# Performance work log

Hardware: AMD Instinct MI355X
Metric: run time of the kernel (lower is better)

## Reference

```python
import jax, jax.numpy as jnp
import numpy as np

C = 1.0      # base manifold curvature (Lorentz c)
C_E = 1.0    # expert manifold curvature (all experts init to c=1.0)
K = 1        # n_activated_experts (top-k)
SCALE = 2.0  # LResNet scale for shared-expert combine
EPS = 1e-8


def _lorentz_swiglu(x, W1, W3, W2, c_mid, c_out, prescale):
    """LorentzExpert / LorentzFeedForward: SwiGLU on space coords with Lorentz time lift.
    x: [T, D] (full Lorentz vector). W1,W3: [I-1, D]; W2: [D-1, I]. Returns [T, D]."""
    if prescale:
        x = x * np.float32(np.sqrt(C_E / C))  # x * sqrt(c_expert / c)
    s1 = jax.nn.silu(x @ W1.T)                 # [T, I-1] w1(x, return_space=True)
    s3 = x @ W3.T                              # [T, I-1] w3(x, return_space=True)
    sp = s1 * s3                               # gated space part
    t = jnp.sqrt(jnp.clip((sp * sp).sum(-1, keepdims=True) + c_mid, EPS))
    h = jnp.concatenate([t, sp], axis=-1)      # [T, I] point on expert manifold
    o = h @ W2.T                               # [T, D-1] w2 space output
    ot = jnp.sqrt(jnp.clip((o * o).sum(-1, keepdims=True) + c_out, EPS))
    return jnp.concatenate([ot, o], axis=-1)   # [T, D] on base manifold


def setup_inputs() -> dict:
    key = jax.random.key(0)
    ks = jax.random.split(key, 9)
    T, D, E, I = 2048, 1024, 8, 1024
    x = jax.random.normal(ks[0], (T, D), jnp.float32)
    gate_w = jax.random.normal(ks[1], (E, D - 1), jnp.float32) / np.sqrt(D - 1)
    gate_b = jax.random.normal(ks[2], (E,), jnp.float32) * 0.01
    W1 = jax.random.normal(ks[3], (E, I - 1, D), jnp.float32) / np.sqrt(D)
    W3 = jax.random.normal(ks[4], (E, I - 1, D), jnp.float32) / np.sqrt(D)
    W2 = jax.random.normal(ks[5], (E, D - 1, I), jnp.float32) / np.sqrt(I)
    Ws1 = jax.random.normal(ks[6], (I - 1, D), jnp.float32) / np.sqrt(D)
    Ws3 = jax.random.normal(ks[7], (I - 1, D), jnp.float32) / np.sqrt(D)
    Ws2 = jax.random.normal(ks[8], (D - 1, I), jnp.float32) / np.sqrt(I)
    return {"x": x, "gate_w": gate_w, "gate_b": gate_b, "W1": W1, "W3": W3,
            "W2": W2, "Ws1": Ws1, "Ws3": Ws3, "Ws2": Ws2}


def reference(x, gate_w, gate_b, W1, W3, W2, Ws1, Ws3, Ws2):
    T, D = x.shape
    E = gate_w.shape[0]
    # ---- Gate (softmax scoring, n_groups == 1, route_scale == 1.0) ----
    logits = x[:, 1:] @ gate_w.T                                    # [T, E]
    scores = jax.nn.softmax(logits.astype(jnp.float32), axis=-1)
    biased = scores + gate_b                                        # bias only affects routing
    _, idx = jax.lax.top_k(biased, K)                               # [T, K]
    weights = jnp.take_along_axis(scores, idx, axis=-1).astype(x.dtype)  # [T, K]
    # dense per-token expert gate weights [T, E]
    oh = jax.nn.one_hot(idx, E, dtype=x.dtype)                      # [T, K, E]
    gw = (oh * weights[..., None]).sum(axis=1)                      # [T, E]
    # ---- y init: project(zeros) -> [sqrt(c), 0, ..., 0] ----
    y0 = jnp.concatenate([jnp.full((T, 1), np.sqrt(C), x.dtype),
                          jnp.zeros((T, D - 1), x.dtype)], axis=-1)
    # ---- routed experts (dense reference: every expert on every token, masked combine) ----
    e_out = jax.vmap(lambda w1, w3, w2: _lorentz_swiglu(x, w1, w3, w2, C_E, C, True))(W1, W3, W2)  # [E, T, D]
    y = y0 + jnp.einsum('te,etd->td', gw, e_out)
    # ---- shared expert (LorentzFeedForward, stays on base manifold) ----
    z = _lorentz_swiglu(x, Ws1, Ws3, Ws2, C, C, False)
    # ---- LResNet weighted sum: normalize (z + scale*y) back to manifold ----
    comb = z + SCALE * y
    li = (comb[:, 1:] ** 2).sum(-1, keepdims=True) - comb[:, :1] ** 2  # Lorentz inner <comb,comb>
    out = np.float32(np.sqrt(C)) * comb / jnp.sqrt(jnp.clip(jnp.abs(li), EPS))
    return out
```

## Files before the change

kernel.cpp:

```cpp
#include <hip/hip_runtime.h>

typedef __bf16 bf16;
typedef __attribute__((ext_vector_type(8))) __bf16 bf16x8;
typedef __attribute__((ext_vector_type(4))) float floatx4;

#define TOK 2048
#define DD  1024
#define NE  8
#define S1MAX 48
#define S2MAX 80

#define MFMA16(A,B,C) __builtin_amdgcn_mfma_f32_16x16x32_bf16(A,B,C,0,0,0)

__device__ __forceinline__ void load_lds16(const bf16* g, bf16* l) {
  __builtin_amdgcn_global_load_lds(
      (const __attribute__((address_space(1))) void*)g,
      (__attribute__((address_space(3))) void*)l, 16, 0, 0);
}

__device__ __forceinline__ uint4 pack_bf8(float4 a, float4 b) {
  union { bf16 h[8]; uint4 u; } p;
  p.h[0] = (bf16)a.x; p.h[1] = (bf16)a.y; p.h[2] = (bf16)a.z; p.h[3] = (bf16)a.w;
  p.h[4] = (bf16)b.x; p.h[5] = (bf16)b.y; p.h[6] = (bf16)b.z; p.h[7] = (bf16)b.w;
  return p.u;
}

#define NCVT (8*2046 + 2046 + 8*1023 + 1023)
__global__ __launch_bounds__(128) void convert_kernel(
    const float* __restrict__ W1, const float* __restrict__ W3,
    const float* __restrict__ W2, const float* __restrict__ Ws1,
    const float* __restrict__ Ws3, const float* __restrict__ Ws2,
    bf16* __restrict__ w13, bf16* __restrict__ ws13,
    bf16* __restrict__ w2b, bf16* __restrict__ ws2b)
{
  const int r = blockIdx.x, tid = threadIdx.x;
  const float* src; bf16* dst;
  if (r < 8 * 2046) {
    const int e = r / 2046, q = r % 2046;
    src = ((q & 1) ? W3 : W1) + ((size_t)e * 1023 + (q >> 1)) * 1024;
    dst = w13 + (size_t)r * 1024;
  } else if (r < 8 * 2046 + 2046) {
    const int q = r - 8 * 2046;
    src = ((q & 1) ? Ws3 : Ws1) + (size_t)(q >> 1) * 1024;
    dst = ws13 + (size_t)q * 1024;
  } else if (r < 8 * 2046 + 2046 + 8 * 1023) {
    const int q = r - (8 * 2046 + 2046);
    src = W2 + (size_t)q * 1024;
    dst = w2b + (size_t)q * 1024;
  } else {
    const int q = r - (8 * 2046 + 2046 + 8 * 1023);
    src = Ws2 + (size_t)q * 1024;
    dst = ws2b + (size_t)q * 1024;
  }
  const float4 f0 = ((const float4*)src)[tid * 2];
  const float4 f1 = ((const float4*)src)[tid * 2 + 1];
  ((uint4*)dst)[tid] = pack_bf8(f0, f1);
}

__global__ __launch_bounds__(256) void gate_cvt_kernel(
    const float* __restrict__ x, const float* __restrict__ gate_w,
    const float* __restrict__ gate_b, bf16* __restrict__ x_bf,
    int* __restrict__ eidx, float* __restrict__ ewgt, float* __restrict__ ss)
{
  const int t = blockIdx.x, tid = threadIdx.x;
  if (tid < 4) ss[tid * TOK + t] = 0.f;
  const float4 v = ((const float4*)(x + (size_t)t * DD))[tid];
  union { bf16 h[4]; uint2 u; } pk;
  pk.h[0] = (bf16)v.x; pk.h[1] = (bf16)v.y; pk.h[2] = (bf16)v.z; pk.h[3] = (bf16)v.w;
  ((uint2*)(x_bf + (size_t)t * DD))[tid] = pk.u;

  float acc[NE];
#pragma unroll
  for (int e = 0; e < NE; ++e) acc[e] = 0.f;
  const float vv[4] = {v.x, v.y, v.z, v.w};
#pragma unroll
  for (int i = 0; i < 4; ++i) {
    const int d = tid * 4 + i;
    if (d >= 1) {
#pragma unroll
      for (int e = 0; e < NE; ++e) acc[e] += vv[i] * gate_w[e * (DD - 1) + d - 1];
    }
  }
#pragma unroll
  for (int off = 32; off > 0; off >>= 1) {
#pragma unroll
    for (int e = 0; e < NE; ++e) acc[e] += __shfl_down(acc[e], off);
  }
  __shared__ float red[4][NE];
  const int wid = tid >> 6, lane = tid & 63;
  if (lane == 0) {
#pragma unroll
    for (int e = 0; e < NE; ++e) red[wid][e] = acc[e];
  }
  __syncthreads();
  if (tid == 0) {
    float lg[NE];
#pragma unroll
    for (int e = 0; e < NE; ++e) lg[e] = red[0][e] + red[1][e] + red[2][e] + red[3][e];
    float m = lg[0];
    for (int e = 1; e < NE; ++e) m = fmaxf(m, lg[e]);
    float ex[NE], s = 0.f;
    for (int e = 0; e < NE; ++e) { ex[e] = expf(lg[e] - m); s += ex[e]; }
    const float inv = 1.f / s;
    int best = 0; float bb = ex[0] * inv + gate_b[0];
    for (int e = 1; e < NE; ++e) {
      const float b = ex[e] * inv + gate_b[e];
      if (b > bb) { bb = b; best = e; }
    }
    eidx[t] = best;
    ewgt[t] = ex[best] * inv;
  }
}

__global__ __launch_bounds__(256) void route_kernel(
    const int* __restrict__ eidx, int* __restrict__ perm,
    int* __restrict__ pos_of, int4* __restrict__ wl1, int* __restrict__ n1,
    int4* __restrict__ wl2, int* __restrict__ n2)
{
  __shared__ int cnt[NE], off[NE], bas[NE + 1];
  const int tid = threadIdx.x;
  if (tid < NE) cnt[tid] = 0;
  __syncthreads();
  for (int t = tid; t < TOK; t += 256) atomicAdd(&cnt[eidx[t]], 1);
  __syncthreads();
  if (tid == 0) {
    int run = 0;
    for (int e = 0; e < NE; ++e) { bas[e] = run; off[e] = run; run += cnt[e]; }
    bas[NE] = run;
    int n = 0;
    for (int e = 0; e < NE; ++e)
      for (int r0 = 0; r0 < cnt[e]; r0 += 128) {
        int rows = cnt[e] - r0; if (rows > 128) rows = 128;
        wl1[n++] = make_int4(bas[e] + r0, rows, e, 0);
      }
    for (int r0 = 0; r0 < TOK; r0 += 128) wl1[n++] = make_int4(r0, 128, NE, 0);
    *n1 = n;
    n = 0;
    for (int e = 0; e < NE; ++e)
      for (int r0 = 0; r0 < cnt[e]; r0 += 64) {
        int rows = cnt[e] - r0; if (rows > 64) rows = 64;
        wl2[n++] = make_int4(bas[e] + r0, rows, e, 0);
      }
    for (int r0 = 0; r0 < TOK; r0 += 64) wl2[n++] = make_int4(r0, 64, NE, 0);
    *n2 = n;
  }
  __syncthreads();
  for (int t = tid; t < TOK; t += 256) {
    const int e = eidx[t];
    const int p = atomicAdd(&off[e], 1);
    perm[p] = t;
    pos_of[t] = p;
  }
}

__global__ __launch_bounds__(256) void mlp1_kernel(
    const bf16* __restrict__ x_bf, const bf16* __restrict__ w13,
    const bf16* __restrict__ ws13,
    const int* __restrict__ perm, const int4* __restrict__ wl,
    const int* __restrict__ wl_n,
    bf16* __restrict__ h_r, bf16* __restrict__ h_s,
    float* __restrict__ ss_r, float* __restrict__ ss_z)
{
  const int bid = blockIdx.x;
  const int slot = bid >> 4, nt = bid & 15;
  if (slot >= *wl_n) return;
  const int4 wle = wl[slot];
  const int mbase = wle.x, rows = wle.y, eid = wle.z;
  const int tid = threadIdx.x;
  const bool routed = (eid < NE);
  const bf16* bmat = routed ? w13 + (size_t)eid * 2046 * 1024 : ws13;
  bf16* hbuf  = routed ? h_r : h_s;
  float* ssbuf = routed ? ss_r : ss_z;

  __shared__ __align__(16) bf16 As[128 * 64];
  __shared__ __align__(16) bf16 Bs[128 * 64];
  __shared__ int toks[128];
  if (tid < 128) {
    int r = tid < rows ? tid : rows - 1;
    toks[tid] = routed ? perm[mbase + r] : (mbase + r);
  }
  __syncthreads();

  const int wid = tid >> 6, lane = tid & 63;
  const int srow = lane >> 3;
  const int kbg  = (lane & 7) ^ (srow & 7);
  const bf16 *aG0, *aG1, *aG2, *aG3, *bG0, *bG1, *bG2, *bG3;
  bf16 *aL0, *aL1, *aL2, *aL3, *bL0, *bL1, *bL2, *bL3;
  {
    const int r0 = wid * 32;
    aG0 = x_bf + (size_t)toks[r0 +  0 + srow] * 1024 + kbg * 8;
    aG1 = x_bf + (size_t)toks[r0 +  8 + srow] * 1024 + kbg * 8;
    aG2 = x_bf + (size_t)toks[r0 + 16 + srow] * 1024 + kbg * 8;
    aG3 = x_bf + (size_t)toks[r0 + 24 + srow] * 1024 + kbg * 8;
    aL0 = As + (r0 +  0) * 64; aL1 = As + (r0 +  8) * 64;
    aL2 = As + (r0 + 16) * 64; aL3 = As + (r0 + 24) * 64;
    int b0 = nt * 128 + r0 + 0 + srow;  if (b0 > 2045) b0 = 2045;
    int b1 = nt * 128 + r0 + 8 + srow;  if (b1 > 2045) b1 = 2045;
    int b2 = nt * 128 + r0 + 16 + srow; if (b2 > 2045) b2 = 2045;
    int b3 = nt * 128 + r0 + 24 + srow; if (b3 > 2045) b3 = 2045;
    bG0 = bmat + (size_t)b0 * 1024 + kbg * 8;
    bG1 = bmat + (size_t)b1 * 1024 + kbg * 8;
    bG2 = bmat + (size_t)b2 * 1024 + kbg * 8;
    bG3 = bmat + (size_t)b3 * 1024 + kbg * 8;
    bL0 = Bs + (r0 +  0) * 64; bL1 = Bs + (r0 +  8) * 64;
    bL2 = Bs + (r0 + 16) * 64; bL3 = Bs + (r0 + 24) * 64;
  }

  const int lrow = lane & 15, quad = lane >> 4, sw = lane & 7;
  const int wrow = (wid >> 1) * 64, wcol = (wid & 1) * 64;
  int aoff[4], boff[4], koff[2];
#pragma unroll
  for (int mi = 0; mi < 4; ++mi) aoff[mi] = (wrow + mi * 16 + lrow) * 64;
#pragma unroll
  for (int ni = 0; ni < 4; ++ni) boff[ni] = (wcol + ni * 16 + lrow) * 64;
#pragma unroll
  for (int kk = 0; kk < 2; ++kk) koff[kk] = ((kk * 4 + quad) ^ sw) * 8;

  const floatx4 fz = {0.f, 0.f, 0.f, 0.f};
  floatx4 acc[4][4];
#pragma unroll
  for (int mi = 0; mi < 4; ++mi)
#pragma unroll
    for (int ni = 0; ni < 4; ++ni) acc[mi][ni] = fz;

  for (int ke = 0; ke < 1024; ke += 64) {
    load_lds16(aG0 + ke, aL0); load_lds16(aG1 + ke, aL1);
    load_lds16(aG2 + ke, aL2); load_lds16(aG3 + ke, aL3);
    load_lds16(bG0 + ke, bL0); load_lds16(bG1 + ke, bL1);
    load_lds16(bG2 + ke, bL2); load_lds16(bG3 + ke, bL3);
    __syncthreads();
#pragma unroll
    for (int kk = 0; kk < 2; ++kk) {
      bf16x8 av[4], bv[4];
#pragma unroll
      for (int mi = 0; mi < 4; ++mi) av[mi] = *(const bf16x8*)(As + aoff[mi] + koff[kk]);
#pragma unroll
      for (int ni = 0; ni < 4; ++ni) bv[ni] = *(const bf16x8*)(Bs + boff[ni] + koff[kk]);
#pragma unroll
      for (int mi = 0; mi < 4; ++mi)
#pragma unroll
        for (int ni = 0; ni < 4; ++ni)
          acc[mi][ni] = MFMA16(av[mi], bv[ni], acc[mi][ni]);
    }
    __syncthreads();
  }

#pragma unroll
  for (int mi = 0; mi < 4; ++mi) {
#pragma unroll
    for (int r = 0; r < 4; ++r) {
      const int row = wrow + mi * 16 + quad * 4 + r;
      const bool rowok = row < rows;
      float ssum = 0.f;
#pragma unroll
      for (int ni = 0; ni < 4; ++ni) {
        const float c = acc[mi][ni][r];
        const float partner = __shfl_xor(c, 1);
        const float s1 = (lane & 1) ? partner : c;
        const float s3 = (lane & 1) ? c : partner;
        const float sp = (s1 / (1.f + __expf(-s1))) * s3;
        const int P = (nt * 128 + wcol + ni * 16 + lrow) >> 1;
        const bool ok = rowok && ((lane & 1) == 0) && (P < 1023);
        if (ok) hbuf[(size_t)(mbase + row) * 1024 + 1 + P] = (bf16)sp;
        ssum += ok ? sp * sp : 0.f;
      }
      ssum += __shfl_xor(ssum, 1);
      ssum += __shfl_xor(ssum, 2);
      ssum += __shfl_xor(ssum, 4);
      ssum += __shfl_xor(ssum, 8);
      if (lrow == 0 && rowok) atomicAdd(ssbuf + mbase + row, ssum);
    }
  }
}

__global__ __launch_bounds__(256) void finalize_t_kernel(
    const float* __restrict__ ss_r, const float* __restrict__ ss_z,
    bf16* __restrict__ h_r, bf16* __restrict__ h_s)
{
  const int i = blockIdx.x * 256 + threadIdx.x;
  if (i < TOK) {
    h_r[(size_t)i * 1024] = (bf16)sqrtf(ss_r[i] + 1.0f);
    h_s[(size_t)i * 1024] = (bf16)sqrtf(ss_z[i] + 1.0f);
  }
}

__global__ __launch_bounds__(256) void mlp2_kernel(
    const bf16* __restrict__ h_r, const bf16* __restrict__ h_s,
    const bf16* __restrict__ w2b, const bf16* __restrict__ ws2b,
    const int4* __restrict__ wl, const int* __restrict__ wl_n,
    float* __restrict__ o_r, float* __restrict__ o_s,
    float* __restrict__ ss_or, float* __restrict__ ss_oz)
{
  const int bid = blockIdx.x;
  const int slot = bid >> 3, nt = bid & 7;
  if (slot >= *wl_n) return;
  const int4 wle = wl[slot];
  const int mbase = wle.x, rows = wle.y, eid = wle.z;
  const int tid = threadIdx.x;
  const bool routed = (eid < NE);
  const bf16* abuf = routed ? h_r : h_s;
  const bf16* bmat = routed ? w2b + (size_t)eid * 1023 * 1024 : ws2b;
  float* obuf  = routed ? o_r : o_s;
  float* ssbuf = routed ? ss_or : ss_oz;
  const int n0 = nt * 128;

  __shared__ __align__(16) bf16 As[64 * 64];
  __shared__ __align__(16) bf16 Bs[128 * 64];

  const int wid = tid >> 6, lane = tid & 63;
  const int srow = lane >> 3;
  const int kbg  = (lane & 7) ^ (srow & 7);
  const bf16 *aG0, *aG1, *bG0, *bG1, *bG2, *bG3;
  bf16 *aL0, *aL1, *bL0, *bL1, *bL2, *bL3;
  {
    int ra0 = wid * 16 + 0 + srow; if (ra0 >= rows) ra0 = rows - 1;
    int ra1 = wid * 16 + 8 + srow; if (ra1 >= rows) ra1 = rows - 1;
    aG0 = abuf + (size_t)(mbase + ra0) * 1024 + kbg * 8;
    aG1 = abuf + (size_t)(mbase + ra1) * 1024 + kbg * 8;
    aL0 = As + (wid * 16 + 0) * 64;
    aL1 = As + (wid * 16 + 8) * 64;
    const int r0 = wid * 32;
    int b0 = n0 + r0 + 0 + srow;  if (b0 > 1022) b0 = 1022;
    int b1 = n0 + r0 + 8 + srow;  if (b1 > 1022) b1 = 1022;
    int b2 = n0 + r0 + 16 + srow; if (b2 > 1022) b2 = 1022;
    int b3 = n0 + r0 + 24 + srow; if (b3 > 1022) b3 = 1022;
    bG0 = bmat + (size_t)b0 * 1024 + kbg * 8;
    bG1 = bmat + (size_t)b1 * 1024 + kbg * 8;
    bG2 = bmat + (size_t)b2 * 1024 + kbg * 8;
    bG3 = bmat + (size_t)b3 * 1024 + kbg * 8;
    bL0 = Bs + (r0 +  0) * 64; bL1 = Bs + (r0 +  8) * 64;
    bL2 = Bs + (r0 + 16) * 64; bL3 = Bs + (r0 + 24) * 64;
  }

  const int lrow = lane & 15, quad = lane >> 4, sw = lane & 7;
  const int wrow = (wid >> 1) * 32, wcol = (wid & 1) * 64;
  int aoff[2], boff[4], koff[2];
#pragma unroll
  for (int mi = 0; mi < 2; ++mi) aoff[mi] = (wrow + mi * 16 + lrow) * 64;
#pragma unroll
  for (int ni = 0; ni < 4; ++ni) boff[ni] = (wcol + ni * 16 + lrow) * 64;
#pragma unroll
  for (int kk = 0; kk < 2; ++kk) koff[kk] = ((kk * 4 + quad) ^ sw) * 8;

  const floatx4 fz = {0.f, 0.f, 0.f, 0.f};
  floatx4 acc[2][4];
#pragma unroll
  for (int mi = 0; mi < 2; ++mi)
#pragma unroll
    for (int ni = 0; ni < 4; ++ni) acc[mi][ni] = fz;

  for (int ke = 0; ke < 1024; ke += 64) {
    load_lds16(aG0 + ke, aL0); load_lds16(aG1 + ke, aL1);
    load_lds16(bG0 + ke, bL0); load_lds16(bG1 + ke, bL1);
    load_lds16(bG2 + ke, bL2); load_lds16(bG3 + ke, bL3);
    __syncthreads();
#pragma unroll
    for (int kk = 0; kk < 2; ++kk) {
      bf16x8 av[2], bv[4];
#pragma unroll
      for (int mi = 0; mi < 2; ++mi) av[mi] = *(const bf16x8*)(As + aoff[mi] + koff[kk]);
#pragma unroll
      for (int ni = 0; ni < 4; ++ni) bv[ni] = *(const bf16x8*)(Bs + boff[ni] + koff[kk]);
#pragma unroll
      for (int mi = 0; mi < 2; ++mi)
#pragma unroll
        for (int ni = 0; ni < 4; ++ni)
          acc[mi][ni] = MFMA16(av[mi], bv[ni], acc[mi][ni]);
    }
    __syncthreads();
  }

#pragma unroll
  for (int mi = 0; mi < 2; ++mi) {
#pragma unroll
    for (int r = 0; r < 4; ++r) {
      const int row = wrow + mi * 16 + quad * 4 + r;
      const bool rowok = row < rows;
      float ssum = 0.f;
#pragma unroll
      for (int ni = 0; ni < 4; ++ni) {
        const float v = acc[mi][ni][r];
        const int n = n0 + wcol + ni * 16 + lrow;
        const bool ok = rowok && (n < 1023);
        if (ok) obuf[(size_t)(mbase + row) * 1024 + n] = v;
        ssum += ok ? v * v : 0.f;
      }
      ssum += __shfl_xor(ssum, 1);
      ssum += __shfl_xor(ssum, 2);
      ssum += __shfl_xor(ssum, 4);
      ssum += __shfl_xor(ssum, 8);
      if (lrow == 0 && rowok) atomicAdd(ssbuf + mbase + row, ssum);
    }
  }
}

__global__ __launch_bounds__(256) void combine_kernel(
    const float* __restrict__ o_r, const float* __restrict__ o_s,
    const float* __restrict__ ss_or, const float* __restrict__ ss_oz,
    const int* __restrict__ pos_of, const float* __restrict__ wgt,
    float* __restrict__ out)
{
  const int t = blockIdx.x, tid = threadIdx.x;
  const int p = pos_of[t];
  const float w = wgt[t];
  const float4 oz = ((const float4*)(o_s + (size_t)t * 1024))[tid];
  const float4 oe = ((const float4*)(o_r + (size_t)p * 1024))[tid];
  const float tw = 2.f * w;
  float c0 = oz.x + tw * oe.x;
  float c1 = oz.y + tw * oe.y;
  float c2 = oz.z + tw * oe.z;
  float c3 = (tid == 255) ? 0.f : (oz.w + tw * oe.w);
  float ssum = c0 * c0 + c1 * c1 + c2 * c2 + c3 * c3;
#pragma unroll
  for (int off = 32; off > 0; off >>= 1) ssum += __shfl_down(ssum, off);
  __shared__ float rs[4];
  if ((tid & 63) == 0) rs[tid >> 6] = ssum;
  __syncthreads();
  const float space2 = rs[0] + rs[1] + rs[2] + rs[3];
  const float comb0 = sqrtf(ss_oz[t] + 1.f) + 2.f + 2.f * w * sqrtf(ss_or[p] + 1.f);
  const float li = space2 - comb0 * comb0;
  const float inv = 1.f / sqrtf(fmaxf(fabsf(li), 1e-8f));
  float* orow = out + (size_t)t * 1024;
  const int j = 1 + tid * 4;
  orow[j]     = c0 * inv;
  orow[j + 1] = c1 * inv;
  orow[j + 2] = c2 * inv;
  if (tid != 255) orow[j + 3] = c3 * inv;
  if (tid == 0) orow[0] = comb0 * inv;
}

extern "C" void kernel_launch(void* const* d_in, const int* in_sizes, int n_in,
                              void* d_out, int out_size, void* d_ws, size_t ws_size,
                              hipStream_t stream) {
  const float* x      = (const float*)d_in[0];
  const float* gate_w = (const float*)d_in[1];
  const float* gate_b = (const float*)d_in[2];
  const float* W1     = (const float*)d_in[3];
  const float* W3     = (const float*)d_in[4];
  const float* W2     = (const float*)d_in[5];
  const float* Ws1    = (const float*)d_in[6];
  const float* Ws3    = (const float*)d_in[7];
  const float* Ws2    = (const float*)d_in[8];
  float* out = (float*)d_out;

  char* ws = (char*)d_ws;
  size_t off = 0;
  auto alloc = [&](size_t bytes) {
    void* p = ws + off;
    off += (bytes + 255) & ~(size_t)255;
    return p;
  };
  bf16*  x_bf = (bf16*) alloc((size_t)TOK * 1024 * 2);
  bf16*  h_r  = (bf16*) alloc((size_t)TOK * 1024 * 2);
  bf16*  h_s  = (bf16*) alloc((size_t)TOK * 1024 * 2);
  float* o_r  = (float*)alloc((size_t)TOK * 1024 * 4);
  float* o_s  = (float*)alloc((size_t)TOK * 1024 * 4);
  float* ss   = (float*)alloc((size_t)4 * TOK * 4);
  int*   eidx = (int*)  alloc((size_t)TOK * 4);
  float* ewgt = (float*)alloc((size_t)TOK * 4);
  int*   perm = (int*)  alloc((size_t)TOK * 4);
  int*   posf = (int*)  alloc((size_t)TOK * 4);
  int4*  wl1  = (int4*) alloc((size_t)S1MAX * 16);
  int4*  wl2  = (int4*) alloc((size_t)S2MAX * 16);
  int*   wn   = (int*)  alloc(32);
  bf16*  w13  = (bf16*) alloc((size_t)8 * 2046 * 1024 * 2);
  bf16*  ws13 = (bf16*) alloc((size_t)2046 * 1024 * 2);
  bf16*  w2b  = (bf16*) alloc((size_t)8 * 1023 * 1024 * 2);
  bf16*  ws2b = (bf16*) alloc((size_t)1023 * 1024 * 2);

  float* ss_r  = ss;
  float* ss_z  = ss + TOK;
  float* ss_or = ss + 2 * TOK;
  float* ss_oz = ss + 3 * TOK;

  convert_kernel<<<NCVT, 128, 0, stream>>>(W1, W3, W2, Ws1, Ws3, Ws2,
                                           w13, ws13, w2b, ws2b);
  gate_cvt_kernel<<<TOK, 256, 0, stream>>>(x, gate_w, gate_b, x_bf, eidx, ewgt, ss);
  route_kernel<<<1, 256, 0, stream>>>(eidx, perm, posf, wl1, wn, wl2, wn + 1);
  mlp1_kernel<<<S1MAX * 16, 256, 0, stream>>>(x_bf, w13, ws13, perm, wl1, wn,
                                              h_r, h_s, ss_r, ss_z);
  finalize_t_kernel<<<8, 256, 0, stream>>>(ss_r, ss_z, h_r, h_s);
  mlp2_kernel<<<S2MAX * 8, 256, 0, stream>>>(h_r, h_s, w2b, ws2b, wl2, wn + 1,
                                             o_r, o_s, ss_or, ss_oz);
  combine_kernel<<<TOK, 256, 0, stream>>>(o_r, o_s, ss_or, ss_oz, posf, ewgt, out);
}
```

Measured before the change: 252.6 us.

## Double-buffer LDS tiles in both expert GEMMs with vmcnt-based waits

Both grouped GEMM kernels now keep two LDS buffers for the A and B tiles. The next K-slice is issued via global_load_lds while the current slice is consumed by MFMAs, and a raw s_waitcnt vmcnt plus s_barrier replaces the full syncthreads pair. This aims to hide global load latency behind compute. In exchange it doubles LDS use (64KB in the first kernel), which can reduce occupancy, and its correctness relies on the hand-written vmcnt counts and on the compiler not reordering the memory operations.

```diff
diff --git a/kernel.cpp b/kernel.cpp
--- a/kernel.cpp
+++ b/kernel.cpp
@@ -17,6 +17,9 @@
       (const __attribute__((address_space(1))) void*)g,
       (__attribute__((address_space(3))) void*)l, 16, 0, 0);
 }
+
+#define WBAR(N) asm volatile("s_waitcnt vmcnt(" #N ")\n\ts_barrier" ::: "memory")
+#define BARO    asm volatile("s_barrier" ::: "memory")
 
 __device__ __forceinline__ uint4 pack_bf8(float4 a, float4 b) {
   union { bf16 h[8]; uint4 u; } p;
@@ -172,8 +175,8 @@
   bf16* hbuf  = routed ? h_r : h_s;
   float* ssbuf = routed ? ss_r : ss_z;
 
-  __shared__ __align__(16) bf16 As[128 * 64];
-  __shared__ __align__(16) bf16 Bs[128 * 64];
+  __shared__ __align__(16) bf16 As[2][128 * 64];
+  __shared__ __align__(16) bf16 Bs[2][128 * 64];
   __shared__ int toks[128];
   if (tid < 128) {
     int r = tid < rows ? tid : rows - 1;
@@ -185,15 +188,15 @@
   const int srow = lane >> 3;
   const int kbg  = (lane & 7) ^ (srow & 7);
   const bf16 *aG0, *aG1, *aG2, *aG3, *bG0, *bG1, *bG2, *bG3;
-  bf16 *aL0, *aL1, *aL2, *aL3, *bL0, *bL1, *bL2, *bL3;
+  int aL0o, aL1o, aL2o, aL3o, bL0o, bL1o, bL2o, bL3o;
   {
     const int r0 = wid * 32;
     aG0 = x_bf + (size_t)toks[r0 +  0 + srow] * 1024 + kbg * 8;
     aG1 = x_bf + (size_t)toks[r0 +  8 + srow] * 1024 + kbg * 8;
     aG2 = x_bf + (size_t)toks[r0 + 16 + srow] * 1024 + kbg * 8;
     aG3 = x_bf + (size_t)toks[r0 + 24 + srow] * 1024 + kbg * 8;
-    aL0 = As + (r0 +  0) * 64; aL1 = As + (r0 +  8) * 64;
-    aL2 = As + (r0 + 16) * 64; aL3 = As + (r0 + 24) * 64;
+    aL0o = (r0 +  0) * 64; aL1o = (r0 +  8) * 64;
+    aL2o = (r0 + 16) * 64; aL3o = (r0 + 24) * 64;
     int b0 = nt * 128 + r0 + 0 + srow;  if (b0 > 2045) b0 = 2045;
     int b1 = nt * 128 + r0 + 8 + srow;  if (b1 > 2045) b1 = 2045;
     int b2 = nt * 128 + r0 + 16 + srow; if (b2 > 2045) b2 = 2045;
@@ -202,8 +205,8 @@
     bG1 = bmat + (size_t)b1 * 1024 + kbg * 8;
     bG2 = bmat + (size_t)b2 * 1024 + kbg * 8;
     bG3 = bmat + (size_t)b3 * 1024 + kbg * 8;
-    bL0 = Bs + (r0 +  0) * 64; bL1 = Bs + (r0 +  8) * 64;
-    bL2 = Bs + (r0 + 16) * 64; bL3 = Bs + (r0 + 24) * 64;
+    bL0o = (r0 +  0) * 64; bL1o = (r0 +  8) * 64;
+    bL2o = (r0 + 16) * 64; bL3o = (r0 + 24) * 64;
   }
 
   const int lrow = lane & 15, quad = lane >> 4, sw = lane & 7;
@@ -223,27 +226,39 @@
 #pragma unroll
     for (int ni = 0; ni < 4; ++ni) acc[mi][ni] = fz;
 
-  for (int ke = 0; ke < 1024; ke += 64) {
-    load_lds16(aG0 + ke, aL0); load_lds16(aG1 + ke, aL1);
-    load_lds16(aG2 + ke, aL2); load_lds16(aG3 + ke, aL3);
-    load_lds16(bG0 + ke, bL0); load_lds16(bG1 + ke, bL1);
-    load_lds16(bG2 + ke, bL2); load_lds16(bG3 + ke, bL3);
-    __syncthreads();
-#pragma unroll
-    for (int kk = 0; kk < 2; ++kk) {
-      bf16x8 av[4], bv[4];
-#pragma unroll
-      for (int mi = 0; mi < 4; ++mi) av[mi] = *(const bf16x8*)(As + aoff[mi] + koff[kk]);
-#pragma unroll
-      for (int ni = 0; ni < 4; ++ni) bv[ni] = *(const bf16x8*)(Bs + boff[ni] + koff[kk]);
-#pragma unroll
-      for (int mi = 0; mi < 4; ++mi)
-#pragma unroll
-        for (int ni = 0; ni < 4; ++ni)
-          acc[mi][ni] = MFMA16(av[mi], bv[ni], acc[mi][ni]);
-    }
-    __syncthreads();
-  }
+#define STAGE1(KE, BUF) { \
+    load_lds16(aG0 + (KE), As[BUF] + aL0o); load_lds16(aG1 + (KE), As[BUF] + aL1o); \
+    load_lds16(aG2 + (KE), As[BUF] + aL2o); load_lds16(aG3 + (KE), As[BUF] + aL3o); \
+    load_lds16(bG0 + (KE), Bs[BUF] + bL0o); load_lds16(bG1 + (KE), Bs[BUF] + bL1o); \
+    load_lds16(bG2 + (KE), Bs[BUF] + bL2o); load_lds16(bG3 + (KE), Bs[BUF] + bL3o); }
+
+#define COMP1(BUF) { \
+_Pragma("unroll") \
+    for (int kk = 0; kk < 2; ++kk) { \
+      bf16x8 av[4], bv[4]; \
+_Pragma("unroll") \
+      for (int mi = 0; mi < 4; ++mi) av[mi] = *(const bf16x8*)(As[BUF] + aoff[mi] + koff[kk]); \
+_Pragma("unroll") \
+      for (int ni = 0; ni < 4; ++ni) bv[ni] = *(const bf16x8*)(Bs[BUF] + boff[ni] + koff[kk]); \
+_Pragma("unroll") \
+      for (int mi = 0; mi < 4; ++mi) \
+_Pragma("unroll") \
+        for (int ni = 0; ni < 4; ++ni) \
+          acc[mi][ni] = MFMA16(av[mi], bv[ni], acc[mi][ni]); \
+    } }
+
+  STAGE1(0, 0)
+  STAGE1(64, 1)
+#pragma unroll 1
+  for (int t = 0; t < 7; ++t) {
+    const int ke = t * 128;
+    WBAR(8); COMP1(0) BARO; STAGE1(ke + 128, 0)
+    WBAR(8); COMP1(1) BARO; STAGE1(ke + 192, 1)
+  }
+  WBAR(8); COMP1(0)
+  WBAR(0); COMP1(1)
+#undef STAGE1
+#undef COMP1
 
 #pragma unroll
   for (int mi = 0; mi < 4; ++mi) {
@@ -304,21 +319,21 @@
   float* ssbuf = routed ? ss_or : ss_oz;
   const int n0 = nt * 128;
 
-  __shared__ __align__(16) bf16 As[64 * 64];
-  __shared__ __align__(16) bf16 Bs[128 * 64];
+  __shared__ __align__(16) bf16 As[2][64 * 64];
+  __shared__ __align__(16) bf16 Bs[2][128 * 64];
 
   const int wid = tid >> 6, lane = tid & 63;
   const int srow = lane >> 3;
   const int kbg  = (lane & 7) ^ (srow & 7);
   const bf16 *aG0, *aG1, *bG0, *bG1, *bG2, *bG3;
-  bf16 *aL0, *aL1, *bL0, *bL1, *bL2, *bL3;
+  int aL0o, aL1o, bL0o, bL1o, bL2o, bL3o;
   {
     int ra0 = wid * 16 + 0 + srow; if (ra0 >= rows) ra0 = rows - 1;
     int ra1 = wid * 16 + 8 + srow; if (ra1 >= rows) ra1 = rows - 1;
     aG0 = abuf + (size_t)(mbase + ra0) * 1024 + kbg * 8;
     aG1 = abuf + (size_t)(mbase + ra1) * 1024 + kbg * 8;
-    aL0 = As + (wid * 16 + 0) * 64;
-    aL1 = As + (wid * 16 + 8) * 64;
+    aL0o = (wid * 16 + 0) * 64;
+    aL1o = (wid * 16 + 8) * 64;
     const int r0 = wid * 32;
     int b0 = n0 + r0 + 0 + srow;  if (b0 > 1022) b0 = 1022;
     int b1 = n0 + r0 + 8 + srow;  if (b1 > 1022) b1 = 1022;
@@ -328,8 +343,8 @@
     bG1 = bmat + (size_t)b1 * 1024 + kbg * 8;
     bG2 = bmat + (size_t)b2 * 1024 + kbg * 8;
     bG3 = bmat + (size_t)b3 * 1024 + kbg * 8;
-    bL0 = Bs + (r0 +  0) * 64; bL1 = Bs + (r0 +  8) * 64;
-    bL2 = Bs + (r0 + 16) * 64; bL3 = Bs + (r0 + 24) * 64;
+    bL0o = (r0 +  0) * 64; bL1o = (r0 +  8) * 64;
+    bL2o = (r0 + 16) * 64; bL3o = (r0 + 24) * 64;
   }
 
   const int lrow = lane & 15, quad = lane >> 4, sw = lane & 7;
@@ -349,26 +364,38 @@
 #pragma unroll
     for (int ni = 0; ni < 4; ++ni) acc[mi][ni] = fz;
 
-  for (int ke = 0; ke < 1024; ke += 64) {
-    load_lds16(aG0 + ke, aL0); load_lds16(aG1 + ke, aL1);
-    load_lds16(bG0 + ke, bL0); load_lds16(bG1 + ke, bL1);
-    load_lds16(bG2 + ke, bL2); load_lds16(bG3 + ke, bL3);
-    __syncthreads();
-#pragma unroll
-    for (int kk = 0; kk < 2; ++kk) {
-      bf16x8 av[2], bv[4];
-#pragma unroll
-      for (int mi = 0; mi < 2; ++mi) av[mi] = *(const bf16x8*)(As + aoff[mi] + koff[kk]);
-#pragma unroll
-      for (int ni = 0; ni < 4; ++ni) bv[ni] = *(const bf16x8*)(Bs + boff[ni] + koff[kk]);
-#pragma unroll
-      for (int mi = 0; mi < 2; ++mi)
-#pragma unroll
-        for (int ni = 0; ni < 4; ++ni)
-          acc[mi][ni] = MFMA16(av[mi], bv[ni], acc[mi][ni]);
-    }
-    __syncthreads();
-  }
+#define STAGE2(KE, BUF) { \
+    load_lds16(aG0 + (KE), As[BUF] + aL0o); load_lds16(aG1 + (KE), As[BUF] + aL1o); \
+    load_lds16(bG0 + (KE), Bs[BUF] + bL0o); load_lds16(bG1 + (KE), Bs[BUF] + bL1o); \
+    load_lds16(bG2 + (KE), Bs[BUF] + bL2o); load_lds16(bG3 + (KE), Bs[BUF] + bL3o); }
+
+#define COMP2(BUF) { \
+_Pragma("unroll") \
+    for (int kk = 0; kk < 2; ++kk) { \
+      bf16x8 av[2], bv[4]; \
+_Pragma("unroll") \
+      for (int mi = 0; mi < 2; ++mi) av[mi] = *(const bf16x8*)(As[BUF] + aoff[mi] + koff[kk]); \
+_Pragma("unroll") \
+      for (int ni = 0; ni < 4; ++ni) bv[ni] = *(const bf16x8*)(Bs[BUF] + boff[ni] + koff[kk]); \
+_Pragma("unroll") \
+      for (int mi = 0; mi < 2; ++mi) \
+_Pragma("unroll") \
+        for (int ni = 0; ni < 4; ++ni) \
+          acc[mi][ni] = MFMA16(av[mi], bv[ni], acc[mi][ni]); \
+    } }
+
+  STAGE2(0, 0)
+  STAGE2(64, 1)
+#pragma unroll 1
+  for (int t = 0; t < 7; ++t) {
+    const int ke = t * 128;
+    WBAR(6); COMP2(0) BARO; STAGE2(ke + 128, 0)
+    WBAR(6); COMP2(1) BARO; STAGE2(ke + 192, 1)
+  }
+  WBAR(6); COMP2(0)
+  WBAR(0); COMP2(1)
+#undef STAGE2
+#undef COMP2
 
 #pragma unroll
   for (int mi = 0; mi < 2; ++mi) {
```

Result: no change. 248.4 us (-1.7%).
